# Kernel optimization log

Measured on AMD Instinct MI355X. Metric: run time of the kernel, lower is better.

## Reference

```python
import jax, jax.numpy as jnp
import numpy as np

B, S, H, W = 16, 512, 768, 8


def _enumerate_spans(S, W):
    # same enumeration order as the torch triple loop: for i, for j in [i, min(i+W, S)-1]
    starts, widths = [], []
    for i in range(S):
        for w in range(1, min(W, S - i) + 1):
            starts.append(i)
            widths.append(w)
    return np.asarray(starts, np.int32), np.asarray(widths, np.int32)


def setup_inputs() -> dict:
    key = jax.random.key(0)
    k1, k2, k3 = jax.random.split(key, 3)
    embeddings = jax.random.normal(k1, (B, S, H), dtype=jnp.float32)
    w_lin = jax.random.normal(k2, (2 * H + 1, H), dtype=jnp.float32) * 0.02
    b_lin = jax.random.normal(k3, (H,), dtype=jnp.float32) * 0.02
    starts, widths = _enumerate_spans(S, W)
    return {
        "embeddings": embeddings,
        "w_lin": w_lin,
        "b_lin": b_lin,
        "span_starts": jnp.asarray(starts),
        "span_widths": jnp.asarray(widths),
    }


def reference(embeddings, w_lin, b_lin, span_starts, span_widths):
    Bb, Ss, Hh = embeddings.shape
    cls_emb = embeddings[:, 0, :]  # [B, H]

    # Sliding-window running max: pooled[k, b, i, :] = max(embeddings[b, i:i+k+1, :])
    neg = jnp.full((Bb, W - 1, Hh), -jnp.inf, embeddings.dtype)
    padded = jnp.concatenate([embeddings, neg], axis=1)  # [B, S+W-1, H]
    cm = embeddings
    pools = [cm]
    for k in range(1, W):
        cm = jnp.maximum(cm, padded[:, k:k + Ss, :])
        pools.append(cm)
    pooled = jnp.stack(pools, axis=0)  # [W, B, S, H]

    # Gather each span's max-pooled embedding: [N, B, H] -> [B, N, H]
    span_max = pooled[span_widths - 1, :, span_starts, :]
    span_max = jnp.transpose(span_max, (1, 0, 2))

    N = span_starts.shape[0]
    cls_b = jnp.broadcast_to(cls_emb[:, None, :], (Bb, N, Hh))
    width_f = jnp.broadcast_to(
        span_widths.astype(embeddings.dtype)[None, :, None], (Bb, N, 1))
    feats = jnp.concatenate([span_max, cls_b, width_f], axis=-1)  # [B, N, 2H+1]

    span_reps = jnp.einsum("bnf,fh->bnh", feats, w_lin) + b_lin
    token_inputs = cls_emb  # [B, H]
    return token_inputs, span_reps.reshape(Bb * N, Hh)
```

## Files before the change

kernel.cpp:

```cpp
#include <hip/hip_runtime.h>
#include <hip/hip_bf16.h>
#include <stdint.h>

typedef float  f32x4  __attribute__((ext_vector_type(4)));
typedef __bf16 bf16x8 __attribute__((ext_vector_type(8)));
typedef __bf16 bf16x4 __attribute__((ext_vector_type(4)));
typedef short  s16x8  __attribute__((ext_vector_type(8)));

static constexpr int Bc = 16, Sc = 512, Hc = 768, NSPAN = 4068;
static constexpr int BM = 128, BN = 256, BK = 64, KS = Hc / BK;

__global__ __launch_bounds__(256)
void prep_w1t(const float* __restrict__ w_lin, unsigned short* __restrict__ w1t) {
  __shared__ __align__(16) unsigned short T[64][80];
  int bidk = blockIdx.x % 12, bidn = blockIdx.x / 12;
  int k0 = bidk * 64, n0 = bidn * 64;
  int tid = threadIdx.x;
#pragma unroll
  for (int p = 0; p < 16; ++p) {
    int idx = p * 256 + tid;
    int kl = idx >> 6, nl = idx & 63;
    float v = w_lin[(size_t)(k0 + kl) * Hc + (n0 + nl)];
    __bf16 bv = (__bf16)v;
    T[nl][kl] = __builtin_bit_cast(unsigned short, bv);
  }
  __syncthreads();
#pragma unroll
  for (int qq = 0; qq < 2; ++qq) {
    int q = qq * 256 + tid;
    int nl = q >> 3, c = q & 7;
    int n = n0 + nl;
    s16x8 v = *(const s16x8*)(&T[nl][c * 8]);
    *(s16x8*)(w1t + (size_t)n * Hc + k0 + c * 8) = v;
  }
}

__global__ __launch_bounds__(256)
void cls_proj_kernel(const float* __restrict__ emb, const float* __restrict__ w_lin,
                     const float* __restrict__ b_lin, float* __restrict__ out,
                     float* __restrict__ cls_proj) {
  __shared__ float cls_s[Hc];
  int b = blockIdx.x / 3, hc = blockIdx.x % 3;
  int tid = threadIdx.x;
  const float* cls = emb + (size_t)b * Sc * Hc;
  for (int i = tid; i < Hc; i += 256) cls_s[i] = cls[i];
  __syncthreads();
  int h = hc * 256 + tid;
  const float* wp = w_lin + (size_t)Hc * Hc + h;
  float p0 = 0, p1 = 0, p2 = 0, p3 = 0, p4 = 0, p5 = 0, p6 = 0, p7 = 0;
  for (int f = 0; f < Hc; f += 8) {
    p0 += cls_s[f + 0] * wp[(size_t)(f + 0) * Hc];
    p1 += cls_s[f + 1] * wp[(size_t)(f + 1) * Hc];
    p2 += cls_s[f + 2] * wp[(size_t)(f + 2) * Hc];
    p3 += cls_s[f + 3] * wp[(size_t)(f + 3) * Hc];
    p4 += cls_s[f + 4] * wp[(size_t)(f + 4) * Hc];
    p5 += cls_s[f + 5] * wp[(size_t)(f + 5) * Hc];
    p6 += cls_s[f + 6] * wp[(size_t)(f + 6) * Hc];
    p7 += cls_s[f + 7] * wp[(size_t)(f + 7) * Hc];
  }
  float acc = b_lin[h] + (((p0 + p1) + (p2 + p3)) + ((p4 + p5) + (p6 + p7)));
  cls_proj[b * Hc + h] = acc;
  out[b * Hc + h] = cls_s[h];
}

__global__ __launch_bounds__(256, 2)
void span_gemm(const float* __restrict__ emb, const unsigned short* __restrict__ w1t,
               const float* __restrict__ cls_proj, const float* __restrict__ w_lin,
               float* __restrict__ out) {
  __shared__ __align__(16) unsigned short Ald[2][BM * BK];

  int bid = blockIdx.x;
  int tile_n = bid % 3, tile_m = bid / 3;
  int b = tile_m >> 5;
  int s0 = (tile_m & 31) << 4;
  int n0 = tile_n * BN;
  int tid = threadIdx.x;
  int wid = tid >> 6, lane = tid & 63;
  int lq = lane >> 4, lr = lane & 15;

  const char* embC = (const char*)(emb + (size_t)b * Sc * Hc);

  int bi = tid >> 4, bkq = tid & 15;
  uint32_t rowoff[8];
#pragma unroll
  for (int t = 0; t < 8; ++t) {
    int r = s0 + bi + t;
    if (r > 511) r = 511;
    rowoff[t] = (uint32_t)r * (Hc * 4) + bkq * 16;
  }
  int awbase = (bi << 10) + ((bkq & 1) << 3);

  const unsigned short* bbase = w1t + (size_t)(n0 + (wid << 6) + lr) * Hc + (lq << 3);

  f32x4 acc[8][4];
  f32x4 zer = {0.f, 0.f, 0.f, 0.f};
#pragma unroll
  for (int i = 0; i < 8; ++i)
#pragma unroll
    for (int j = 0; j < 4; ++j) acc[i][j] = zer;

  f32x4 rv[8];
  bf16x8 bfr[4][2];

#define BUILD_A(dstbuf)                                                        \
  {                                                                            \
    f32x4 cm = rv[0];                                                          \
    _Pragma("unroll") for (int t = 0; t < 8; ++t) {                            \
      if (t) {                                                                 \
        cm[0] = fmaxf(cm[0], rv[t][0]);                                        \
        cm[1] = fmaxf(cm[1], rv[t][1]);                                        \
        cm[2] = fmaxf(cm[2], rv[t][2]);                                        \
        cm[3] = fmaxf(cm[3], rv[t][3]);                                        \
      }                                                                        \
      bf16x4 p;                                                                \
      p[0] = (__bf16)cm[0]; p[1] = (__bf16)cm[1];                              \
      p[2] = (__bf16)cm[2]; p[3] = (__bf16)cm[3];                              \
      int off = awbase + (t << 7) + ((((bkq >> 1) ^ t)) << 4);                 \
      *(uint2*)((char*)(dstbuf) + off) = __builtin_bit_cast(uint2, p);         \
    }                                                                          \
  }

#pragma unroll
  for (int t = 0; t < 8; ++t) rv[t] = *(const f32x4*)(embC + rowoff[t]);
  BUILD_A(Ald[0]);
#pragma unroll
  for (int t = 0; t < 8; ++t) rv[t] = *(const f32x4*)(embC + rowoff[t] + 256);
#pragma unroll
  for (int ni = 0; ni < 4; ++ni)
#pragma unroll
    for (int kk = 0; kk < 2; ++kk)
      bfr[ni][kk] = *(const bf16x8*)(bbase + ni * 16 * Hc + kk * 32);
  asm volatile("s_waitcnt lgkmcnt(0)" ::: "memory");
  __builtin_amdgcn_sched_barrier(0);
  __builtin_amdgcn_s_barrier();

  for (int ks = 0; ks < KS; ++ks) {
    const char* abuf = (const char*)Ald[ks & 1];
#pragma unroll
    for (int kk = 0; kk < 2; ++kk) {
      bf16x8 af[8];
      int cf = (kk << 2) + lq;
#pragma unroll
      for (int mi = 0; mi < 8; ++mi) {
        int m = (mi << 4) + lr;
        af[mi] = *(const bf16x8*)(abuf + (m << 7) + ((cf ^ (m & 7)) << 4));
      }
#pragma unroll
      for (int mi = 0; mi < 8; ++mi)
#pragma unroll
        for (int ni = 0; ni < 4; ++ni)
          acc[mi][ni] = __builtin_amdgcn_mfma_f32_16x16x32_bf16(af[mi], bfr[ni][kk], acc[mi][ni], 0, 0, 0);
    }

    if (ks < KS - 1) {
      BUILD_A(Ald[(ks + 1) & 1]);
      if (ks < KS - 2) {
#pragma unroll
        for (int t = 0; t < 8; ++t)
          rv[t] = *(const f32x4*)(embC + rowoff[t] + (ks + 2) * 256);
      }
#pragma unroll
      for (int ni = 0; ni < 4; ++ni)
#pragma unroll
        for (int kk = 0; kk < 2; ++kk)
          bfr[ni][kk] = *(const bf16x8*)(bbase + ni * 16 * Hc + (ks + 1) * 64 + kk * 32);
      asm volatile("s_waitcnt lgkmcnt(0)" ::: "memory");
      __builtin_amdgcn_sched_barrier(0);
      __builtin_amdgcn_s_barrier();
    }
  }

  const float* w2p = w_lin + (size_t)(2 * Hc) * Hc;
  float* outp = out + Bc * Hc;
  int swb = (tile_m & 31) << 7;
#pragma unroll
  for (int ni = 0; ni < 4; ++ni) {
    int h = n0 + (wid << 6) + (ni << 4) + lr;
    float cp = cls_proj[b * Hc + h];
    float w2 = w2p[h];
#pragma unroll
    for (int mi = 0; mi < 8; ++mi) {
#pragma unroll
      for (int j = 0; j < 4; ++j) {
        int m = (mi << 4) + (lq << 2) + j;
        int sw = swb + m;
        int s = sw >> 3, w = (sw & 7) + 1;
        if (s + w <= 512) {
          int nsp = (s <= 504) ? (sw)
                               : (NSPAN - (((512 - s) * (513 - s)) >> 1) + w - 1);
          size_t oidx = ((size_t)b * NSPAN + nsp) * Hc + h;
          outp[oidx] = acc[mi][ni][j] + cp + (float)w * w2;
        }
      }
    }
  }
}

extern "C" void kernel_launch(void* const* d_in, const int* in_sizes, int n_in,
                              void* d_out, int out_size, void* d_ws, size_t ws_size,
                              hipStream_t stream) {
  const float* emb = (const float*)d_in[0];
  const float* w_lin = (const float*)d_in[1];
  const float* b_lin = (const float*)d_in[2];
  unsigned short* w1t = (unsigned short*)d_ws;
  float* cls_proj = (float*)((char*)d_ws + (size_t)Hc * Hc * 2);
  float* out = (float*)d_out;

  hipLaunchKernelGGL(prep_w1t, dim3(144), dim3(256), 0, stream, w_lin, w1t);
  hipLaunchKernelGGL(cls_proj_kernel, dim3(48), dim3(256), 0, stream, emb, w_lin, b_lin, out, cls_proj);
  hipLaunchKernelGGL(span_gemm, dim3(512 * 3), dim3(256), 0, stream, emb, w1t, cls_proj, w_lin, out);
}
```

Measured before the change: 150.2 us.

## Stage B tiles in LDS via global_load_lds with 2x2 wave tiling

```diff
diff --git a/kernel.cpp b/kernel.cpp
--- a/kernel.cpp
+++ b/kernel.cpp
@@ -1,6 +1,9 @@
 #include <hip/hip_runtime.h>
 #include <hip/hip_bf16.h>
 #include <stdint.h>
+
+#define AS1 __attribute__((address_space(1)))
+#define AS3 __attribute__((address_space(3)))
 
 typedef float  f32x4  __attribute__((ext_vector_type(4)));
 typedef __bf16 bf16x8 __attribute__((ext_vector_type(8)));
@@ -8,7 +11,7 @@
 typedef short  s16x8  __attribute__((ext_vector_type(8)));
 
 static constexpr int Bc = 16, Sc = 512, Hc = 768, NSPAN = 4068;
-static constexpr int BM = 128, BN = 256, BK = 64, KS = Hc / BK;
+static constexpr int BM = 128, BN = 128, BK = 64, KS = Hc / BK;
 
 __global__ __launch_bounds__(256)
 void prep_w1t(const float* __restrict__ w_lin, unsigned short* __restrict__ w1t) {
@@ -30,8 +33,9 @@
     int q = qq * 256 + tid;
     int nl = q >> 3, c = q & 7;
     int n = n0 + nl;
+    int gp = (k0 >> 3) + (c ^ (n & 7));
     s16x8 v = *(const s16x8*)(&T[nl][c * 8]);
-    *(s16x8*)(w1t + (size_t)n * Hc + k0 + c * 8) = v;
+    *(s16x8*)(w1t + (size_t)n * Hc + gp * 8) = v;
   }
 }
 
@@ -68,14 +72,17 @@
                const float* __restrict__ cls_proj, const float* __restrict__ w_lin,
                float* __restrict__ out) {
   __shared__ __align__(16) unsigned short Ald[2][BM * BK];
-
-  int bid = blockIdx.x;
-  int tile_n = bid % 3, tile_m = bid / 3;
+  __shared__ __align__(16) unsigned short Bld[2][BN * BK];
+
+  int wg = blockIdx.x;
+  int wgid = (wg & 7) * 384 + (wg >> 3);
+  int tile_n = wgid % 6, tile_m = wgid / 6;
   int b = tile_m >> 5;
   int s0 = (tile_m & 31) << 4;
-  int n0 = tile_n * BN;
+  int n0 = tile_n << 7;
   int tid = threadIdx.x;
   int wid = tid >> 6, lane = tid & 63;
+  int wave_m = wid >> 1, wave_n = wid & 1;
   int lq = lane >> 4, lr = lane & 15;
 
   const char* embC = (const char*)(emb + (size_t)b * Sc * Hc);
@@ -90,17 +97,18 @@
   }
   int awbase = (bi << 10) + ((bkq & 1) << 3);
 
-  const unsigned short* bbase = w1t + (size_t)(n0 + (wid << 6) + lr) * Hc + (lq << 3);
-
-  f32x4 acc[8][4];
+  f32x4 acc[4][4];
   f32x4 zer = {0.f, 0.f, 0.f, 0.f};
 #pragma unroll
-  for (int i = 0; i < 8; ++i)
+  for (int i = 0; i < 4; ++i)
 #pragma unroll
     for (int j = 0; j < 4; ++j) acc[i][j] = zer;
 
   f32x4 rv[8];
-  bf16x8 bfr[4][2];
+
+#define LOAD_RV(koff)                                                          \
+  _Pragma("unroll") for (int t = 0; t < 8; ++t)                                \
+      rv[t] = *(const f32x4*)(embC + rowoff[t] + (koff));
 
 #define BUILD_A(dstbuf)                                                        \
   {                                                                            \
@@ -120,77 +128,85 @@
     }                                                                          \
   }
 
-#pragma unroll
-  for (int t = 0; t < 8; ++t) rv[t] = *(const f32x4*)(embC + rowoff[t]);
+#define GLL_B(k0, dstbuf)                                                      \
+  _Pragma("unroll") for (int j = 0; j < 4; ++j) {                              \
+    int u = (wid << 2) + j;                                                    \
+    int n = n0 + (u << 3) + (lane >> 3);                                       \
+    const unsigned short* gp = w1t + (size_t)n * Hc + (k0) + ((lane & 7) << 3);\
+    __builtin_amdgcn_global_load_lds((const AS1 uint32_t*)gp,                  \
+                                     (AS3 uint32_t*)((dstbuf) + (u << 9)), 16, 0, 0); \
+  }
+
+#define MFMA_STEP(buf)                                                         \
+  _Pragma("unroll") for (int kk = 0; kk < 2; ++kk) {                           \
+    bf16x8 af[4], bfr[4];                                                      \
+    int cf = (kk << 2) + lq;                                                   \
+    _Pragma("unroll") for (int mi = 0; mi < 4; ++mi) {                         \
+      int m = (wave_m << 6) + (mi << 4) + lr;                                  \
+      af[mi] = *(const bf16x8*)((const char*)Ald[buf] + (m << 7) + ((cf ^ (m & 7)) << 4)); \
+    }                                                                          \
+    _Pragma("unroll") for (int ni = 0; ni < 4; ++ni) {                         \
+      int n = (wave_n << 6) + (ni << 4) + lr;                                  \
+      bfr[ni] = *(const bf16x8*)((const char*)Bld[buf] + (n << 7) + ((cf ^ (n & 7)) << 4)); \
+    }                                                                          \
+    _Pragma("unroll") for (int mi = 0; mi < 4; ++mi)                           \
+      _Pragma("unroll") for (int ni = 0; ni < 4; ++ni)                         \
+        acc[mi][ni] = __builtin_amdgcn_mfma_f32_16x16x32_bf16(af[mi], bfr[ni], acc[mi][ni], 0, 0, 0); \
+  }
+
+  LOAD_RV(0);
   BUILD_A(Ald[0]);
-#pragma unroll
-  for (int t = 0; t < 8; ++t) rv[t] = *(const f32x4*)(embC + rowoff[t] + 256);
-#pragma unroll
-  for (int ni = 0; ni < 4; ++ni)
-#pragma unroll
-    for (int kk = 0; kk < 2; ++kk)
-      bfr[ni][kk] = *(const bf16x8*)(bbase + ni * 16 * Hc + kk * 32);
-  asm volatile("s_waitcnt lgkmcnt(0)" ::: "memory");
+  GLL_B(0, Bld[0]);
+  LOAD_RV(256);
+
+  for (int ks = 0; ks < KS - 1; ++ks) {
+    asm volatile("s_waitcnt vmcnt(8) lgkmcnt(0)" ::: "memory");
+    __builtin_amdgcn_sched_barrier(0);
+    __builtin_amdgcn_s_barrier();
+    __builtin_amdgcn_sched_barrier(0);
+
+    int nb = (ks + 1) & 1;
+    BUILD_A(Ald[nb]);
+    GLL_B((ks + 1) * BK, Bld[nb]);
+    {
+      int kn = (ks + 2 < KS) ? (ks + 2) : (KS - 1);
+      LOAD_RV(kn * 256);
+    }
+    MFMA_STEP(ks & 1);
+  }
+
+  asm volatile("s_waitcnt vmcnt(0) lgkmcnt(0)" ::: "memory");
   __builtin_amdgcn_sched_barrier(0);
   __builtin_amdgcn_s_barrier();
-
-  for (int ks = 0; ks < KS; ++ks) {
-    const char* abuf = (const char*)Ald[ks & 1];
-#pragma unroll
-    for (int kk = 0; kk < 2; ++kk) {
-      bf16x8 af[8];
-      int cf = (kk << 2) + lq;
-#pragma unroll
-      for (int mi = 0; mi < 8; ++mi) {
-        int m = (mi << 4) + lr;
-        af[mi] = *(const bf16x8*)(abuf + (m << 7) + ((cf ^ (m & 7)) << 4));
-      }
-#pragma unroll
-      for (int mi = 0; mi < 8; ++mi)
-#pragma unroll
-        for (int ni = 0; ni < 4; ++ni)
-          acc[mi][ni] = __builtin_amdgcn_mfma_f32_16x16x32_bf16(af[mi], bfr[ni][kk], acc[mi][ni], 0, 0, 0);
-    }
-
-    if (ks < KS - 1) {
-      BUILD_A(Ald[(ks + 1) & 1]);
-      if (ks < KS - 2) {
-#pragma unroll
-        for (int t = 0; t < 8; ++t)
-          rv[t] = *(const f32x4*)(embC + rowoff[t] + (ks + 2) * 256);
-      }
-#pragma unroll
-      for (int ni = 0; ni < 4; ++ni)
-#pragma unroll
-        for (int kk = 0; kk < 2; ++kk)
-          bfr[ni][kk] = *(const bf16x8*)(bbase + ni * 16 * Hc + (ks + 1) * 64 + kk * 32);
-      asm volatile("s_waitcnt lgkmcnt(0)" ::: "memory");
-      __builtin_amdgcn_sched_barrier(0);
-      __builtin_amdgcn_s_barrier();
-    }
-  }
+  __builtin_amdgcn_sched_barrier(0);
+  MFMA_STEP((KS - 1) & 1);
 
   const float* w2p = w_lin + (size_t)(2 * Hc) * Hc;
   float* outp = out + Bc * Hc;
   int swb = (tile_m & 31) << 7;
+  float cp[4], w2[4];
 #pragma unroll
   for (int ni = 0; ni < 4; ++ni) {
-    int h = n0 + (wid << 6) + (ni << 4) + lr;
-    float cp = cls_proj[b * Hc + h];
-    float w2 = w2p[h];
-#pragma unroll
-    for (int mi = 0; mi < 8; ++mi) {
-#pragma unroll
-      for (int j = 0; j < 4; ++j) {
-        int m = (mi << 4) + (lq << 2) + j;
-        int sw = swb + m;
-        int s = sw >> 3, w = (sw & 7) + 1;
-        if (s + w <= 512) {
-          int nsp = (s <= 504) ? (sw)
-                               : (NSPAN - (((512 - s) * (513 - s)) >> 1) + w - 1);
-          size_t oidx = ((size_t)b * NSPAN + nsp) * Hc + h;
-          outp[oidx] = acc[mi][ni][j] + cp + (float)w * w2;
-        }
+    int h = n0 + (wave_n << 6) + (ni << 4) + lr;
+    cp[ni] = cls_proj[b * Hc + h];
+    w2[ni] = w2p[h];
+  }
+  int hbase = n0 + (wave_n << 6) + lr;
+#pragma unroll
+  for (int mi = 0; mi < 4; ++mi) {
+#pragma unroll
+    for (int j = 0; j < 4; ++j) {
+      int m = (wave_m << 6) + (mi << 4) + (lq << 2) + j;
+      int sw = swb + m;
+      int s = sw >> 3, w = (sw & 7) + 1;
+      if (s + w <= 512) {
+        int nsp = (s <= 504) ? sw
+                             : (NSPAN - (((512 - s) * (513 - s)) >> 1) + w - 1);
+        float* rowp = outp + ((size_t)b * NSPAN + nsp) * Hc + hbase;
+        float wf = (float)w;
+#pragma unroll
+        for (int ni = 0; ni < 4; ++ni)
+          rowp[ni << 4] = acc[mi][ni][j] + cp[ni] + wf * w2[ni];
       }
     }
   }
@@ -208,5 +224,5 @@
 
   hipLaunchKernelGGL(prep_w1t, dim3(144), dim3(256), 0, stream, w_lin, w1t);
   hipLaunchKernelGGL(cls_proj_kernel, dim3(48), dim3(256), 0, stream, emb, w_lin, b_lin, out, cls_proj);
-  hipLaunchKernelGGL(span_gemm, dim3(512 * 3), dim3(256), 0, stream, emb, w1t, cls_proj, w_lin, out);
-}
+  hipLaunchKernelGGL(span_gemm, dim3(512 * 6), dim3(256), 0, stream, emb, w1t, cls_proj, w_lin, out);
+}
```

Measured after the change: 142.9 us. 1.05x faster.
